# Kernel tuning notes

Hardware: AMD Instinct MI355X
Metric: run time of the kernel (lower is better)

The kernel has to match this reference:

```python
import jax, jax.numpy as jnp
import numpy as np

B, M, E = 8192, 200, 64
OTHER = 128
FEA = 256  # E + E + OTHER
ADIM = 3 * E


def setup_inputs() -> dict:
    key = jax.random.key(0)
    ks = jax.random.split(key, 12)
    s = lambda fan: 1.0 / np.sqrt(fan)
    return {
        "hist": jax.random.normal(ks[0], (B, M, E), jnp.float32),
        "target": jax.random.normal(ks[1], (B, E), jnp.float32),
        "other": jax.random.normal(ks[2], (B, OTHER), jnp.float32),
        "aW1": jax.random.normal(ks[3], (ADIM, ADIM // 2), jnp.float32) * s(ADIM),
        "ab1": jnp.zeros((ADIM // 2,), jnp.float32),
        "aW2": jax.random.normal(ks[4], (ADIM // 2, 1), jnp.float32) * s(ADIM // 2),
        "ab2": jnp.zeros((1,), jnp.float32),
        "oW1": jax.random.normal(ks[5], (FEA, FEA // 2), jnp.float32) * s(FEA),
        "ob1": jnp.zeros((FEA // 2,), jnp.float32),
        "oW2": jax.random.normal(ks[6], (FEA // 2, FEA // 3), jnp.float32) * s(FEA // 2),
        "ob2": jnp.zeros((FEA // 3,), jnp.float32),
        "oW3": jax.random.normal(ks[7], (FEA // 3, FEA // 4), jnp.float32) * s(FEA // 3),
        "ob3": jnp.zeros((FEA // 4,), jnp.float32),
        "fW": jax.random.normal(ks[8], (FEA // 4, 1), jnp.float32) * s(FEA // 4),
        "fb": jnp.zeros((1,), jnp.float32),
    }


def reference(hist, target, other, aW1, ab1, aW2, ab2,
              oW1, ob1, oW2, ob2, oW3, ob3, fW, fb):
    # DIN activation unit, vectorized over the m history steps.
    tgt = target[:, None, :]                                  # [B,1,E]
    a = jnp.concatenate(
        [hist, hist * tgt, jnp.broadcast_to(tgt, hist.shape)], axis=-1
    )                                                          # [B,M,3E]
    h = jax.nn.relu(jnp.einsum("bma,ah->bmh", a, aW1) + ab1)   # [B,M,3E/2]
    aij = jnp.einsum("bmh,ho->bmo", h, aW2) + ab2              # [B,M,1]
    tmp = jnp.sum(aij * hist, axis=1)                          # [B,E]

    x = jnp.concatenate([tmp, target, other], axis=1)          # [B,FEA]
    x = jax.nn.relu(x @ oW1 + ob1)
    x = jax.nn.relu(x @ oW2 + ob2)
    x = jax.nn.relu(x @ oW3 + ob3)
    out = jax.nn.sigmoid(x @ fW + fb)                          # [B,1]
    return out
```

## Files before the change

### kernel.cpp

```cpp
#include <hip/hip_runtime.h>
#include <math.h>

#define BATCH 8192
#define M 200
#define E 64
#define H1 96
#define F1 128
#define F2 85
#define F3 64
#define SH 72
#define MT 13

typedef _Float16 half8_t __attribute__((ext_vector_type(8)));
typedef float floatx4 __attribute__((ext_vector_type(4)));

__global__ __launch_bounds__(256, 4) void din_kernel(
    const float* __restrict__ hist, const float* __restrict__ target,
    const float* __restrict__ other,
    const float* __restrict__ aW1, const float* __restrict__ ab1,
    const float* __restrict__ aW2, const float* __restrict__ ab2,
    const float* __restrict__ oW1, const float* __restrict__ ob1,
    const float* __restrict__ oW2, const float* __restrict__ ob2,
    const float* __restrict__ oW3, const float* __restrict__ ob3,
    const float* __restrict__ fW,  const float* __restrict__ fb,
    float* __restrict__ out)
{
    __shared__ _Float16 WbT[H1 * SH];
    __shared__ float tgtS[E];
    __shared__ float beS[H1];
    __shared__ float aW2S[H1];
    __shared__ float partS[4 * E];
    __shared__ float xS[256];
    __shared__ float h1p[256];
    __shared__ float h1S[F1];
    __shared__ float h2p[256];
    __shared__ float h2S[F2];
    __shared__ float h3S[F3];
    __shared__ float ab2S;

    const int t = threadIdx.x;
    const int b = blockIdx.x;

    if (t < E) tgtS[t] = target[(size_t)b * E + t];
    if (t == 0) ab2S = ab2[0];
    __syncthreads();

    for (int idx = t; idx < E * H1; idx += 256) {
        int k = idx / H1, j = idx - k * H1;
        float w = aW1[idx] + tgtS[k] * aW1[E * H1 + idx];
        WbT[j * SH + k] = (_Float16)w;
    }
    if (t < H1) {
        float s = ab1[t];
        for (int k = 0; k < E; ++k)
            s += tgtS[k] * aW1[(2 * E + k) * H1 + t];
        beS[t] = s;
        aW2S[t] = aW2[t];
    }
    __syncthreads();

    const int lane = t & 63;
    const int wv   = t >> 6;
    const int quad = lane >> 4;
    const int lm   = lane & 15;

    half8_t bf[12];
    #pragma unroll
    for (int nt = 0; nt < 6; ++nt) {
        #pragma unroll
        for (int kk = 0; kk < 2; ++kk)
            bf[nt * 2 + kk] =
                *(const half8_t*)&WbT[(nt * 16 + lm) * SH + kk * 32 + quad * 8];
    }

    float tk0[8], tk1[8];
    #pragma unroll
    for (int j = 0; j < 8; ++j) { tk0[j] = 0.f; tk1[j] = 0.f; }

    const int qs16 = (lm >> 2) << 4;
    const int rsel = lm & 3;

    for (int mt = wv; mt < MT; mt += 4) {
        const int m0 = mt * 16;
        const int row = m0 + lm;
        const int rowc = row < M ? row : (M - 1);
        const float4* p = (const float4*)(hist + ((size_t)b * M + rowc) * E + quad * 8);
        float4 f0 = p[0], g0 = p[1];
        float4 f1 = p[8], g1 = p[9];
        half8_t a0 = { (_Float16)f0.x, (_Float16)f0.y, (_Float16)f0.z, (_Float16)f0.w,
                       (_Float16)g0.x, (_Float16)g0.y, (_Float16)g0.z, (_Float16)g0.w };
        half8_t a1 = { (_Float16)f1.x, (_Float16)f1.y, (_Float16)f1.z, (_Float16)f1.w,
                       (_Float16)g1.x, (_Float16)g1.y, (_Float16)g1.z, (_Float16)g1.w };

        float s0 = 0.f, s1 = 0.f, s2 = 0.f, s3 = 0.f;
        #pragma unroll
        for (int nt = 0; nt < 6; ++nt) {
            floatx4 acc = {0.f, 0.f, 0.f, 0.f};
            acc = __builtin_amdgcn_mfma_f32_16x16x32_f16(a0, bf[nt * 2],     acc, 0, 0, 0);
            acc = __builtin_amdgcn_mfma_f32_16x16x32_f16(a1, bf[nt * 2 + 1], acc, 0, 0, 0);
            float be_n = beS[nt * 16 + lm];
            float w2   = aW2S[nt * 16 + lm];
            s0 += fmaxf(acc[0] + be_n, 0.f) * w2;
            s1 += fmaxf(acc[1] + be_n, 0.f) * w2;
            s2 += fmaxf(acc[2] + be_n, 0.f) * w2;
            s3 += fmaxf(acc[3] + be_n, 0.f) * w2;
        }
        #pragma unroll
        for (int off = 1; off < 16; off <<= 1) {
            s0 += __shfl_xor(s0, off);
            s1 += __shfl_xor(s1, off);
            s2 += __shfl_xor(s2, off);
            s3 += __shfl_xor(s3, off);
        }
        float v0 = __shfl(s0, qs16), v1 = __shfl(s1, qs16);
        float v2 = __shfl(s2, qs16), v3 = __shfl(s3, qs16);
        float aij = (rsel == 0) ? v0 : (rsel == 1) ? v1 : (rsel == 2) ? v2 : v3;
        aij += ab2S;
        aij = (row < M) ? aij : 0.f;

        tk0[0] += f0.x * aij; tk0[1] += f0.y * aij;
        tk0[2] += f0.z * aij; tk0[3] += f0.w * aij;
        tk0[4] += g0.x * aij; tk0[5] += g0.y * aij;
        tk0[6] += g0.z * aij; tk0[7] += g0.w * aij;
        tk1[0] += f1.x * aij; tk1[1] += f1.y * aij;
        tk1[2] += f1.z * aij; tk1[3] += f1.w * aij;
        tk1[4] += g1.x * aij; tk1[5] += g1.y * aij;
        tk1[6] += g1.z * aij; tk1[7] += g1.w * aij;
    }

    #pragma unroll
    for (int j = 0; j < 8; ++j) {
        #pragma unroll
        for (int off = 1; off < 16; off <<= 1) {
            tk0[j] += __shfl_xor(tk0[j], off);
            tk1[j] += __shfl_xor(tk1[j], off);
        }
    }
    if (lm == 0) {
        #pragma unroll
        for (int j = 0; j < 8; ++j) {
            partS[wv * E + quad * 8 + j]      = tk0[j];
            partS[wv * E + 32 + quad * 8 + j] = tk1[j];
        }
    }
    __syncthreads();

    if (t < 64)
        xS[t] = partS[t] + partS[64 + t] + partS[128 + t] + partS[192 + t];
    else if (t < 128)
        xS[t] = tgtS[t - 64];
    else
        xS[t] = other[(size_t)b * 128 + (t - 128)];
    __syncthreads();

    {
        int j = t & 127, ph = t >> 7;
        float s = ph ? 0.f : ob1[j];
        const float* w = oW1 + (size_t)(ph * 128) * F1 + j;
        int c0 = ph * 128;
        for (int c = 0; c < 128; ++c)
            s += xS[c0 + c] * w[(size_t)c * F1];
        h1p[ph * 128 + j] = s;
    }
    __syncthreads();
    if (t < F1) h1S[t] = fmaxf(h1p[t] + h1p[128 + t], 0.f);
    __syncthreads();

    {
        int o = t & 127, ph = t >> 7;
        if (o < F2) {
            float s = ph ? 0.f : ob2[o];
            int c0 = ph * 64;
            for (int c = c0; c < c0 + 64; ++c)
                s += h1S[c] * oW2[(size_t)c * F2 + o];
            h2p[ph * 128 + o] = s;
        }
    }
    __syncthreads();
    if (t < F2) h2S[t] = fmaxf(h2p[t] + h2p[128 + t], 0.f);
    __syncthreads();

    if (t < F3) {
        float s = ob3[t];
        for (int c = 0; c < F2; ++c)
            s += h2S[c] * oW3[(size_t)c * F3 + t];
        h3S[t] = fmaxf(s, 0.f);
    }
    __syncthreads();

    if (t < 64) {
        float v = h3S[t] * fW[t];
        v += __shfl_xor(v, 1);  v += __shfl_xor(v, 2);  v += __shfl_xor(v, 4);
        v += __shfl_xor(v, 8);  v += __shfl_xor(v, 16); v += __shfl_xor(v, 32);
        if (t == 0) out[b] = 1.f / (1.f + __expf(-(v + fb[0])));
    }
}

extern "C" void kernel_launch(void* const* d_in, const int* in_sizes, int n_in,
                              void* d_out, int out_size, void* d_ws, size_t ws_size,
                              hipStream_t stream) {
    const float* hist   = (const float*)d_in[0];
    const float* target = (const float*)d_in[1];
    const float* other  = (const float*)d_in[2];
    const float* aW1    = (const float*)d_in[3];
    const float* ab1    = (const float*)d_in[4];
    const float* aW2    = (const float*)d_in[5];
    const float* ab2    = (const float*)d_in[6];
    const float* oW1    = (const float*)d_in[7];
    const float* ob1    = (const float*)d_in[8];
    const float* oW2    = (const float*)d_in[9];
    const float* ob2    = (const float*)d_in[10];
    const float* oW3    = (const float*)d_in[11];
    const float* ob3    = (const float*)d_in[12];
    const float* fW     = (const float*)d_in[13];
    const float* fb     = (const float*)d_in[14];
    float* out = (float*)d_out;

    din_kernel<<<BATCH, 256, 0, stream>>>(hist, target, other,
                                          aW1, ab1, aW2, ab2,
                                          oW1, ob1, oW2, ob2, oW3, ob3,
                                          fW, fb, out);
}
```

Before: 746.3 us.

## Prefetch hist tiles, cache bias in registers, and split MLP tails across all threads

```diff
diff --git a/kernel.cpp b/kernel.cpp
--- a/kernel.cpp
+++ b/kernel.cpp
@@ -29,17 +29,28 @@
     __shared__ float tgtS[E];
     __shared__ float beS[H1];
     __shared__ float aW2S[H1];
-    __shared__ float partS[4 * E];
     __shared__ float xS[256];
-    __shared__ float h1p[256];
+    __shared__ float scr[512];
     __shared__ float h1S[F1];
-    __shared__ float h2p[256];
     __shared__ float h2S[F2];
-    __shared__ float h3S[F3];
     __shared__ float ab2S;
 
     const int t = threadIdx.x;
     const int b = blockIdx.x;
+    const int lane = t & 63;
+    const int wv   = t >> 6;
+    const int quad = lane >> 4;
+    const int lm   = lane & 15;
+
+    {
+    }
+    int mt = wv;
+    const int row0  = mt * 16 + lm;
+    const int rowc0 = row0 < M ? row0 : (M - 1);
+    const float4* p0 = (const float4*)(hist + ((size_t)b * M + rowc0) * E + quad * 8);
+    float4 f0 = p0[0], g0 = p0[1], f1 = p0[8], g1 = p0[9];
+    float oth = 0.f;
+    if (t >= 128) oth = other[(size_t)b * 128 + (t - 128)];
 
     if (t < E) tgtS[t] = target[(size_t)b * E + t];
     if (t == 0) ab2S = ab2[0];
@@ -51,18 +62,19 @@
         WbT[j * SH + k] = (_Float16)w;
     }
     if (t < H1) {
-        float s = ab1[t];
-        for (int k = 0; k < E; ++k)
-            s += tgtS[k] * aW1[(2 * E + k) * H1 + t];
-        beS[t] = s;
+        float s0 = ab1[t], s1 = 0.f, s2 = 0.f, s3 = 0.f;
+        const float* wp = aW1 + (size_t)(2 * E) * H1 + t;
+        #pragma unroll 4
+        for (int k = 0; k < E; k += 4) {
+            s0 += tgtS[k]     * wp[(size_t)k * H1];
+            s1 += tgtS[k + 1] * wp[(size_t)(k + 1) * H1];
+            s2 += tgtS[k + 2] * wp[(size_t)(k + 2) * H1];
+            s3 += tgtS[k + 3] * wp[(size_t)(k + 3) * H1];
+        }
+        beS[t] = (s0 + s1) + (s2 + s3);
         aW2S[t] = aW2[t];
     }
     __syncthreads();
-
-    const int lane = t & 63;
-    const int wv   = t >> 6;
-    const int quad = lane >> 4;
-    const int lm   = lane & 15;
 
     half8_t bf[12];
     #pragma unroll
@@ -72,6 +84,12 @@
             bf[nt * 2 + kk] =
                 *(const half8_t*)&WbT[(nt * 16 + lm) * SH + kk * 32 + quad * 8];
     }
+    float beR[6], w2R[6];
+    #pragma unroll
+    for (int nt = 0; nt < 6; ++nt) {
+        beR[nt] = beS[nt * 16 + lm];
+        w2R[nt] = aW2S[nt * 16 + lm];
+    }
 
     float tk0[8], tk1[8];
     #pragma unroll
@@ -80,13 +98,18 @@
     const int qs16 = (lm >> 2) << 4;
     const int rsel = lm & 3;
 
-    for (int mt = wv; mt < MT; mt += 4) {
-        const int m0 = mt * 16;
+    for (; mt < MT; mt += 4) {
+        const int nmt = mt + 4;
+        float4 nf0 = f0, ng0 = g0, nf1 = f1, ng1 = g1;
+        if (nmt < MT) {
+            const int nrow  = nmt * 16 + lm;
+            const int nrowc = nrow < M ? nrow : (M - 1);
+            const float4* np = (const float4*)(hist + ((size_t)b * M + nrowc) * E + quad * 8);
+            nf0 = np[0]; ng0 = np[1]; nf1 = np[8]; ng1 = np[9];
+        }
+
+        const int m0  = mt * 16;
         const int row = m0 + lm;
-        const int rowc = row < M ? row : (M - 1);
-        const float4* p = (const float4*)(hist + ((size_t)b * M + rowc) * E + quad * 8);
-        float4 f0 = p[0], g0 = p[1];
-        float4 f1 = p[8], g1 = p[9];
         half8_t a0 = { (_Float16)f0.x, (_Float16)f0.y, (_Float16)f0.z, (_Float16)f0.w,
                        (_Float16)g0.x, (_Float16)g0.y, (_Float16)g0.z, (_Float16)g0.w };
         half8_t a1 = { (_Float16)f1.x, (_Float16)f1.y, (_Float16)f1.z, (_Float16)f1.w,
@@ -98,8 +121,8 @@
             floatx4 acc = {0.f, 0.f, 0.f, 0.f};
             acc = __builtin_amdgcn_mfma_f32_16x16x32_f16(a0, bf[nt * 2],     acc, 0, 0, 0);
             acc = __builtin_amdgcn_mfma_f32_16x16x32_f16(a1, bf[nt * 2 + 1], acc, 0, 0, 0);
-            float be_n = beS[nt * 16 + lm];
-            float w2   = aW2S[nt * 16 + lm];
+            float be_n = beR[nt];
+            float w2   = w2R[nt];
             s0 += fmaxf(acc[0] + be_n, 0.f) * w2;
             s1 += fmaxf(acc[1] + be_n, 0.f) * w2;
             s2 += fmaxf(acc[2] + be_n, 0.f) * w2;
@@ -126,6 +149,8 @@
         tk1[2] += f1.z * aij; tk1[3] += f1.w * aij;
         tk1[4] += g1.x * aij; tk1[5] += g1.y * aij;
         tk1[6] += g1.z * aij; tk1[7] += g1.w * aij;
+
+        f0 = nf0; g0 = ng0; f1 = nf1; g1 = ng1;
     }
 
     #pragma unroll
@@ -139,57 +164,76 @@
     if (lm == 0) {
         #pragma unroll
         for (int j = 0; j < 8; ++j) {
-            partS[wv * E + quad * 8 + j]      = tk0[j];
-            partS[wv * E + 32 + quad * 8 + j] = tk1[j];
+            scr[wv * E + quad * 8 + j]      = tk0[j];
+            scr[wv * E + 32 + quad * 8 + j] = tk1[j];
         }
     }
     __syncthreads();
 
     if (t < 64)
-        xS[t] = partS[t] + partS[64 + t] + partS[128 + t] + partS[192 + t];
+        xS[t] = (scr[t] + scr[64 + t]) + (scr[128 + t] + scr[192 + t]);
     else if (t < 128)
         xS[t] = tgtS[t - 64];
     else
-        xS[t] = other[(size_t)b * 128 + (t - 128)];
-    __syncthreads();
-
-    {
-        int j = t & 127, ph = t >> 7;
-        float s = ph ? 0.f : ob1[j];
-        const float* w = oW1 + (size_t)(ph * 128) * F1 + j;
-        int c0 = ph * 128;
-        for (int c = 0; c < 128; ++c)
-            s += xS[c0 + c] * w[(size_t)c * F1];
-        h1p[ph * 128 + j] = s;
-    }
-    __syncthreads();
-    if (t < F1) h1S[t] = fmaxf(h1p[t] + h1p[128 + t], 0.f);
-    __syncthreads();
-
-    {
-        int o = t & 127, ph = t >> 7;
+        xS[t] = oth;
+    __syncthreads();
+
+    {
+        const int g = t & 31, s = t >> 5;
+        const float* wbase = oW1 + 4 * g;
+        const int c0 = s * 32;
+        float ax = 0.f, ay = 0.f, az = 0.f, aw = 0.f;
+        #pragma unroll 8
+        for (int i = 0; i < 32; ++i) {
+            const int c = c0 + i;
+            float xv = xS[c];
+            float4 w4 = *(const float4*)(wbase + (size_t)c * F1);
+            ax += xv * w4.x; ay += xv * w4.y;
+            az += xv * w4.z; aw += xv * w4.w;
+        }
+        ax += __shfl_xor(ax, 32);
+        ay += __shfl_xor(ay, 32);
+        az += __shfl_xor(az, 32);
+        aw += __shfl_xor(aw, 32);
+        if (lane < 32) {
+            float4 r = { ax, ay, az, aw };
+            *(float4*)&scr[wv * 128 + 4 * g] = r;
+        }
+    }
+    __syncthreads();
+    if (t < F1)
+        h1S[t] = fmaxf((scr[t] + scr[128 + t]) + (scr[256 + t] + scr[384 + t]) + ob1[t], 0.f);
+    __syncthreads();
+
+    {
+        const int o = t & 127, ph = t >> 7;
         if (o < F2) {
-            float s = ph ? 0.f : ob2[o];
-            int c0 = ph * 64;
-            for (int c = c0; c < c0 + 64; ++c)
-                s += h1S[c] * oW2[(size_t)c * F2 + o];
-            h2p[ph * 128 + o] = s;
-        }
-    }
-    __syncthreads();
-    if (t < F2) h2S[t] = fmaxf(h2p[t] + h2p[128 + t], 0.f);
-    __syncthreads();
-
-    if (t < F3) {
-        float s = ob3[t];
-        for (int c = 0; c < F2; ++c)
-            s += h2S[c] * oW3[(size_t)c * F3 + t];
-        h3S[t] = fmaxf(s, 0.f);
+            float sA = 0.f, sB = 0.f;
+            const int c0 = ph * 64;
+            #pragma unroll 8
+            for (int c = 0; c < 64; c += 2) {
+                sA += h1S[c0 + c]     * oW2[(size_t)(c0 + c) * F2 + o];
+                sB += h1S[c0 + c + 1] * oW2[(size_t)(c0 + c + 1) * F2 + o];
+            }
+            scr[ph * 128 + o] = sA + sB;
+        }
+    }
+    __syncthreads();
+    if (t < F2) h2S[t] = fmaxf(scr[t] + scr[128 + t] + ob2[t], 0.f);
+    __syncthreads();
+
+    {
+        const int o = t & 63, ph = t >> 6;
+        const int c0 = (85 * ph) >> 2, c1 = (85 * (ph + 1)) >> 2;
+        float s = 0.f;
+        for (int c = c0; c < c1; ++c)
+            s += h2S[c] * oW3[(size_t)c * F3 + o];
+        scr[ph * 64 + o] = s;
     }
     __syncthreads();
 
     if (t < 64) {
-        float v = h3S[t] * fW[t];
+        float v = fmaxf((scr[t] + scr[64 + t]) + (scr[128 + t] + scr[192 + t]) + ob3[t], 0.f) * fW[t];
         v += __shfl_xor(v, 1);  v += __shfl_xor(v, 2);  v += __shfl_xor(v, 4);
         v += __shfl_xor(v, 8);  v += __shfl_xor(v, 16); v += __shfl_xor(v, 32);
         if (t == 0) out[b] = 1.f / (1.f + __expf(-(v + fb[0])));
```

New measurement: 743.9 us. No clear change (-0.3%).
